# Kernel tuning notes

Hardware: AMD Instinct MI355X
Metric: run time of the kernel (lower is better)

Reference implementation:

```python
import jax, jax.numpy as jnp
import numpy as np

B, S, INPUT_DIM = 8, 2048, 512
D_MODEL, N_LAYERS, OUTPUT_DIM = 1024, 6, 512
LAMBDA_INIT = 0.5


def _sinusoidal_pe(seq_len, d_model):
    # standard sinusoidal positional encoding, added over the sequence dim
    pos = np.arange(seq_len, dtype=np.float32)[:, None]
    div = np.exp(-np.log(10000.0) * np.arange(0, d_model, 2, dtype=np.float32) / d_model)
    pe = np.zeros((seq_len, d_model), dtype=np.float32)
    pe[:, 0::2] = np.sin(pos * div)
    pe[:, 1::2] = np.cos(pos * div)
    return jnp.asarray(pe)


def setup_inputs() -> dict:
    key = jax.random.key(0)
    ks = jax.random.split(key, 10)
    scale = 0.02
    x = jax.random.normal(ks[0], (B, S, INPUT_DIM), dtype=jnp.float32)
    W_in = jax.random.normal(ks[1], (D_MODEL, INPUT_DIM), dtype=jnp.float32) * scale
    b_in = jnp.zeros((D_MODEL,), dtype=jnp.float32)
    W_ctx = jax.random.normal(ks[2], (D_MODEL, D_MODEL), dtype=jnp.float32) * scale
    b_ctx = jnp.zeros((D_MODEL,), dtype=jnp.float32)
    # per-layer in_proj splits: W_q, W_k, W_v each [d_model, d_model]
    Wq = jax.random.normal(ks[3], (N_LAYERS, D_MODEL, D_MODEL), dtype=jnp.float32) * scale
    Wk = jax.random.normal(ks[4], (N_LAYERS, D_MODEL, D_MODEL), dtype=jnp.float32) * scale
    Wv = jax.random.normal(ks[5], (N_LAYERS, D_MODEL, D_MODEL), dtype=jnp.float32) * scale
    W_out = jax.random.normal(ks[6], (OUTPUT_DIM, D_MODEL), dtype=jnp.float32) * scale
    b_out = jnp.zeros((OUTPUT_DIM,), dtype=jnp.float32)
    return {"x": x, "W_in": W_in, "b_in": b_in, "W_ctx": W_ctx, "b_ctx": b_ctx,
            "Wq": Wq, "Wk": Wk, "Wv": Wv, "W_out": W_out, "b_out": b_out}


def _diff_attention(h, W_q, W_k, W_v):
    # h: [B, S, d]; weights used un-transposed, matching X @ W_q in the source
    d = h.shape[-1]
    half = d // 2
    Q = h @ W_q
    K = h @ W_k
    V = h @ W_v
    Q1, Q2 = Q[..., :half], Q[..., half:]
    K1, K2 = K[..., :half], K[..., half:]
    s = 1.0 / jnp.sqrt(jnp.float32(d))
    A1 = jnp.einsum('bqd,bkd->bqk', Q1, K1) * s  # [B, S, S]
    A2 = jnp.einsum('bqd,bkd->bqk', Q2, K2) * s
    scores = jax.nn.softmax(A1, axis=-1) - LAMBDA_INIT * jax.nn.softmax(A2, axis=-1)
    return jnp.einsum('bqk,bkd->bqd', scores, V)


def reference(x, W_in, b_in, W_ctx, b_ctx, Wq, Wk, Wv, W_out, b_out):
    h = x @ W_in.T + b_in            # input_fc
    h = h @ W_ctx.T + b_ctx          # context_embedding
    h = h + _sinusoidal_pe(S, D_MODEL)[None, :, :]
    for i in range(N_LAYERS):
        h = _diff_attention(h, Wq[i], Wk[i], Wv[i])
    return h @ W_out.T + b_out
```

## Files before the change

### kernel.cpp

```cpp
#include <hip/hip_runtime.h>
#include <stdint.h>

typedef unsigned short u16b;
typedef __attribute__((ext_vector_type(8))) __bf16 bf16x8;
typedef __attribute__((ext_vector_type(8))) unsigned short ushort8;
typedef __attribute__((ext_vector_type(4))) float f32x4;

#define B_    8
#define S_    2048
#define DIN_  512
#define DM_   1024
#define NL_   6
#define DOUT_ 512
#define MTOT  (B_ * S_)

__device__ __forceinline__ u16b f2bf(float f) {
  unsigned u = __builtin_bit_cast(unsigned, f);
  u += 0x7fffu + ((u >> 16) & 1u);
  return (u16b)(u >> 16);
}
__device__ __forceinline__ float bf2f(u16b h) {
  return __builtin_bit_cast(float, (unsigned)h << 16);
}

__global__ void pe_kernel(float* __restrict__ pe) {
  int idx = blockIdx.x * 256 + threadIdx.x;
  int s = idx >> 10, d = idx & 1023;
  int j = d >> 1;
  double div = exp(-log(10000.0) * (double)(2 * j) / 1024.0);
  double ang = (double)s * div;
  pe[idx] = (float)((d & 1) ? cos(ang) : sin(ang));
}

__global__ void cvt_bf16(const float* __restrict__ in, u16b* __restrict__ out, long long n) {
  long long i = (long long)blockIdx.x * 256 + threadIdx.x;
  long long st = (long long)gridDim.x * 256;
  for (; i < n; i += st) out[i] = f2bf(in[i]);
}

__global__ __launch_bounds__(256) void tr3v2(const float* __restrict__ q,
                                             const float* __restrict__ k,
                                             const float* __restrict__ v,
                                             u16b* __restrict__ oq, u16b* __restrict__ ok2,
                                             u16b* __restrict__ ov) {
  __shared__ float tile[64 * 65];
  const float* in = blockIdx.z == 0 ? q : (blockIdx.z == 1 ? k : v);
  u16b* out = blockIdx.z == 0 ? oq : (blockIdx.z == 1 ? ok2 : ov);
  int c0 = blockIdx.x * 64, r0 = blockIdx.y * 64;
  int t = threadIdx.x;
#pragma unroll
  for (int i = 0; i < 4; ++i) {
    int id = i * 256 + t;
    int r = id >> 4, cq = (id & 15) * 4;
    float4 val = *(const float4*)&in[(size_t)(r0 + r) * DM_ + c0 + cq];
    tile[r * 65 + cq + 0] = val.x;
    tile[r * 65 + cq + 1] = val.y;
    tile[r * 65 + cq + 2] = val.z;
    tile[r * 65 + cq + 3] = val.w;
  }
  __syncthreads();
#pragma unroll
  for (int i = 0; i < 2; ++i) {
    int id = i * 256 + t;
    int c = id >> 3, rq = (id & 7) * 8;
    ushort8 o;
#pragma unroll
    for (int j = 0; j < 8; ++j) o[j] = f2bf(tile[(rq + j) * 65 + c]);
    *(ushort8*)&out[(size_t)(c0 + c) * DM_ + r0 + rq] = o;
  }
}

__global__ __launch_bounds__(256) void softmax_combine(const float* __restrict__ A1,
                                                       const float* __restrict__ A2,
                                                       u16b* __restrict__ P,
                                                       long long pstride) {
  size_t row = blockIdx.x;
  const float* a1 = A1 + row * 2048;
  const float* a2 = A2 + row * 2048;
  u16b* p = P + row * pstride;
  int t = threadIdx.x, w = t >> 6, lane = t & 63;
  float v1[8], v2[8];
  float m1 = -3.4e38f, m2 = -3.4e38f;
#pragma unroll
  for (int i = 0; i < 8; ++i) {
    v1[i] = a1[i * 256 + t];
    v2[i] = a2[i * 256 + t];
    m1 = fmaxf(m1, v1[i]);
    m2 = fmaxf(m2, v2[i]);
  }
  __shared__ float red1[4], red2[4];
#pragma unroll
  for (int o = 32; o; o >>= 1) {
    m1 = fmaxf(m1, __shfl_xor(m1, o));
    m2 = fmaxf(m2, __shfl_xor(m2, o));
  }
  if (lane == 0) { red1[w] = m1; red2[w] = m2; }
  __syncthreads();
  m1 = fmaxf(fmaxf(red1[0], red1[1]), fmaxf(red1[2], red1[3]));
  m2 = fmaxf(fmaxf(red2[0], red2[1]), fmaxf(red2[2], red2[3]));
  float s1 = 0.f, s2 = 0.f;
#pragma unroll
  for (int i = 0; i < 8; ++i) {
    v1[i] = expf(v1[i] - m1);
    v2[i] = expf(v2[i] - m2);
    s1 += v1[i];
    s2 += v2[i];
  }
#pragma unroll
  for (int o = 32; o; o >>= 1) {
    s1 += __shfl_xor(s1, o);
    s2 += __shfl_xor(s2, o);
  }
  __syncthreads();
  if (lane == 0) { red1[w] = s1; red2[w] = s2; }
  __syncthreads();
  s1 = red1[0] + red1[1] + red1[2] + red1[3];
  s2 = red2[0] + red2[1] + red2[2] + red2[3];
  float i1 = 1.0f / s1, i2 = 0.5f / s2;
#pragma unroll
  for (int i = 0; i < 8; ++i)
    p[i * 256 + t] = f2bf(v1[i] * i1 - v2[i] * i2);
}

__global__ __launch_bounds__(256) void softmax_full(u16b* __restrict__ A1b,
                                                    const u16b* __restrict__ A2b) {
  size_t ro = (size_t)blockIdx.x * S_;
  u16b* a1 = A1b + ro;
  const u16b* a2 = A2b + ro;
  int t = threadIdx.x, w = t >> 6, lane = t & 63;
  ushort8 x1 = *(const ushort8*)&a1[t * 8];
  ushort8 x2 = *(const ushort8*)&a2[t * 8];
  float v1[8], v2[8];
  float m1 = -3.4e38f, m2 = -3.4e38f;
#pragma unroll
  for (int i = 0; i < 8; ++i) {
    v1[i] = bf2f(x1[i]);
    v2[i] = bf2f(x2[i]);
    m1 = fmaxf(m1, v1[i]);
    m2 = fmaxf(m2, v2[i]);
  }
  __shared__ float red1[4], red2[4];
#pragma unroll
  for (int o = 32; o; o >>= 1) {
    m1 = fmaxf(m1, __shfl_xor(m1, o));
    m2 = fmaxf(m2, __shfl_xor(m2, o));
  }
  if (lane == 0) { red1[w] = m1; red2[w] = m2; }
  __syncthreads();
  m1 = fmaxf(fmaxf(red1[0], red1[1]), fmaxf(red1[2], red1[3]));
  m2 = fmaxf(fmaxf(red2[0], red2[1]), fmaxf(red2[2], red2[3]));
  float s1 = 0.f, s2 = 0.f;
#pragma unroll
  for (int i = 0; i < 8; ++i) {
    v1[i] = expf(v1[i] - m1);
    v2[i] = expf(v2[i] - m2);
    s1 += v1[i];
    s2 += v2[i];
  }
#pragma unroll
  for (int o = 32; o; o >>= 1) {
    s1 += __shfl_xor(s1, o);
    s2 += __shfl_xor(s2, o);
  }
  __syncthreads();
  if (lane == 0) { red1[w] = s1; red2[w] = s2; }
  __syncthreads();
  s1 = red1[0] + red1[1] + red1[2] + red1[3];
  s2 = red2[0] + red2[1] + red2[2] + red2[3];
  float i1 = 1.0f / s1, i2 = 0.5f / s2;
  ushort8 outv;
#pragma unroll
  for (int i = 0; i < 8; ++i) outv[i] = f2bf(v1[i] * i1 - v2[i] * i2);
  *(ushort8*)&a1[t * 8] = outv;
}

#define GEPI_BF16      0
#define GEPI_BIAS      1
#define GEPI_BIAS_PE   2
#define GEPI_F32SCALE  3
#define GEPI_F32BIAS   4
#define GEPI_BF16_VT   5
#define GEPI_BF16SCALE 6
#define GEPI_QKV       7

template <int EPI>
__global__ __launch_bounds__(256) void gemm_nt(
    const u16b* __restrict__ A, long long sAr, long long sAb,
    const u16b* __restrict__ Bt, long long sBr, long long sBb,
    void* __restrict__ Cv, long long sCr, long long sCb,
    int K, const float* __restrict__ bias, const float* __restrict__ pe, float alpha) {
  __shared__ __align__(16) u16b smem[16384];
  u16b* As = smem;
  u16b* Bs = smem + 8192;
  const int z = blockIdx.z;
  const u16b* Ab = A + (size_t)z * sAb;
  const u16b* Bb = Bt + (size_t)z * sBb;
  const int m0 = blockIdx.x * 128, n0 = blockIdx.y * 128;
  const int t = threadIdx.x;
  const int w = t >> 6, lane = t & 63;
  const int wr = w >> 1, wc = w & 1;
  const int lr = lane & 15, g0 = lane >> 4;

  f32x4 acc[4][4] = {};

  const int nkt = K >> 6;
  for (int kt = 0; kt < nkt; ++kt) {
#pragma unroll
    for (int i = 0; i < 4; ++i) {
      int c = i * 256 + t;
      int r = c >> 3, cc = c & 7;
      int gc = cc ^ (r & 7);
      const u16b* ga = Ab + (size_t)(m0 + r) * sAr + kt * 64 + gc * 8;
      const u16b* gb = Bb + (size_t)(n0 + r) * sBr + kt * 64 + gc * 8;
      u16b* la = &As[(i * 256 + w * 64) * 8];
      u16b* lb = &Bs[(i * 256 + w * 64) * 8];
      __builtin_amdgcn_global_load_lds((__attribute__((address_space(1))) void*)ga,
                                       (__attribute__((address_space(3))) void*)la, 16, 0, 0);
      __builtin_amdgcn_global_load_lds((__attribute__((address_space(1))) void*)gb,
                                       (__attribute__((address_space(3))) void*)lb, 16, 0, 0);
    }
    __syncthreads();
#pragma unroll
    for (int kk = 0; kk < 2; ++kk) {
      bf16x8 af[4], bfr[4];
#pragma unroll
      for (int m = 0; m < 4; ++m) {
        int r = wr * 64 + m * 16 + lr;
        int sidx = (kk * 4 + g0) ^ (r & 7);
        af[m] = *(const bf16x8*)&As[(r * 8 + sidx) * 8];
      }
#pragma unroll
      for (int n = 0; n < 4; ++n) {
        int r = wc * 64 + n * 16 + lr;
        int sidx = (kk * 4 + g0) ^ (r & 7);
        bfr[n] = *(const bf16x8*)&Bs[(r * 8 + sidx) * 8];
      }
#pragma unroll
      for (int m = 0; m < 4; ++m)
#pragma unroll
        for (int n = 0; n < 4; ++n)
          acc[m][n] = __builtin_amdgcn_mfma_f32_16x16x32_bf16(af[m], bfr[n], acc[m][n], 0, 0, 0);
    }
    __syncthreads();
  }

  u16b* Ch = (u16b*)Cv;
  float* Cf = (float*)Cv;
  const size_t cb = (size_t)z * sCb;
#pragma unroll
  for (int m = 0; m < 4; ++m) {
#pragma unroll
    for (int j = 0; j < 4; ++j) {
      int r = m0 + wr * 64 + m * 16 + g0 * 4 + j;
      size_t ro = cb + (size_t)r * sCr;
#pragma unroll
      for (int n = 0; n < 4; ++n) {
        int c = n0 + wc * 64 + n * 16 + lr;
        float v = acc[m][n][j];
        if constexpr (EPI == GEPI_BF16) Ch[ro + c] = f2bf(v);
        else if constexpr (EPI == GEPI_BIAS) Ch[ro + c] = f2bf(v + bias[c]);
        else if constexpr (EPI == GEPI_BIAS_PE)
          Ch[ro + c] = f2bf(v + bias[c] + pe[(size_t)(r & (S_ - 1)) * DM_ + c]);
        else if constexpr (EPI == GEPI_F32SCALE) Cf[ro + c] = v * alpha;
        else Cf[ro + c] = v + bias[c];
      }
    }
  }
}

template <int EPI>
__global__ __launch_bounds__(512, 1) void gemm8(
    const u16b* __restrict__ A, long long sAr, long long sAb, long long sAb2,
    const u16b* __restrict__ Bt, long long sBr, long long sBb, long long sBb2,
    void* __restrict__ Cv, long long sCr, long long sCb, long long sCb2,
    int K, const float* __restrict__ bias, const float* __restrict__ pe, float alpha) {
  extern __shared__ __align__(16) u16b lds[];
  const int z = blockIdx.z;
  const u16b* Ab = A + (size_t)(z >> 1) * sAb2 + (size_t)(z & 1) * sAb;
  const u16b* Bb = Bt + (size_t)(z >> 1) * sBb2 + (size_t)(z & 1) * sBb;
  const int m0 = blockIdx.x * 256, n0 = blockIdx.y * 256;
  const int t = threadIdx.x;
  const int wid = t >> 6, lane = t & 63;
  const int wr = wid >> 2, wc = wid & 3;
  const int lr = lane & 15, g0 = lane >> 4;

  f32x4 acc[8][4] = {};
  const int nkt = K >> 6;

  auto stage = [&](int kt, int buf) {
    u16b* bufA = lds + buf * 32768;
    u16b* bufB = bufA + 16384;
#pragma unroll
    for (int i = 0; i < 4; ++i) {
      int id = i * 512 + t;
      int r = id >> 3, cc = id & 7;
      int gc = cc ^ (r & 7);
      const u16b* ga = Ab + (size_t)(m0 + r) * sAr + kt * 64 + gc * 8;
      const u16b* gb = Bb + (size_t)(n0 + r) * sBr + kt * 64 + gc * 8;
      u16b* la = bufA + (i * 512 + wid * 64) * 8;
      u16b* lb = bufB + (i * 512 + wid * 64) * 8;
      __builtin_amdgcn_global_load_lds((__attribute__((address_space(1))) void*)ga,
                                       (__attribute__((address_space(3))) void*)la, 16, 0, 0);
      __builtin_amdgcn_global_load_lds((__attribute__((address_space(1))) void*)gb,
                                       (__attribute__((address_space(3))) void*)lb, 16, 0, 0);
    }
  };

  stage(0, 0);
  __builtin_amdgcn_sched_barrier(0);
  asm volatile("s_waitcnt vmcnt(0)" ::: "memory");
  __builtin_amdgcn_sched_barrier(0);
  __builtin_amdgcn_s_barrier();
  __builtin_amdgcn_sched_barrier(0);

  for (int kt = 0; kt < nkt; ++kt) {
    const int cur = kt & 1;
    if (kt + 1 < nkt) stage(kt + 1, cur ^ 1);
    __builtin_amdgcn_sched_barrier(0);
    const u16b* bufA = lds + cur * 32768;
    const u16b* bufB = bufA + 16384;
#pragma unroll
    for (int kk = 0; kk < 2; ++kk) {
      bf16x8 af[8], bfr[4];
#pragma unroll
      for (int m = 0; m < 8; ++m) {
        int r = wr * 128 + m * 16 + lr;
        int sidx = (kk * 4 + g0) ^ (r & 7);
        af[m] = *(const bf16x8*)&bufA[(r * 8 + sidx) * 8];
      }
#pragma unroll
      for (int n = 0; n < 4; ++n) {
        int r = wc * 64 + n * 16 + lr;
        int sidx = (kk * 4 + g0) ^ (r & 7);
        bfr[n] = *(const bf16x8*)&bufB[(r * 8 + sidx) * 8];
      }
      __builtin_amdgcn_s_setprio(1);
#pragma unroll
      for (int m = 0; m < 8; ++m)
#pragma unroll
        for (int n = 0; n < 4; ++n)
          acc[m][n] = __builtin_amdgcn_mfma_f32_16x16x32_bf16(af[m], bfr[n], acc[m][n], 0, 0, 0);
      __builtin_amdgcn_s_setprio(0);
    }
    __builtin_amdgcn_sched_barrier(0);
    asm volatile("s_waitcnt vmcnt(0)" ::: "memory");
    __builtin_amdgcn_sched_barrier(0);
    __builtin_amdgcn_s_barrier();
    __builtin_amdgcn_sched_barrier(0);
  }

  const bool doVT = (EPI == GEPI_BF16_VT) || (EPI == GEPI_QKV && z == 2);
  if (doVT) {
    u16b* tile = lds;
    u16b* vtb = (EPI == GEPI_QKV) ? (u16b*)(void*)pe : (u16b*)Cv;
#pragma unroll
    for (int m = 0; m < 8; ++m)
#pragma unroll
      for (int j = 0; j < 4; ++j) {
        int rl = wr * 128 + m * 16 + g0 * 4 + j;
#pragma unroll
        for (int n = 0; n < 4; ++n) {
          int cl = wc * 64 + n * 16 + lr;
          tile[cl * 256 + (rl ^ ((cl & 7) << 3))] = f2bf(acc[m][n][j]);
        }
      }
    __syncthreads();
    const int batch = m0 >> 11;
    const int r0b = m0 & (S_ - 1);
    u16b* obase = vtb + (size_t)batch * DM_ * S_ + r0b;
#pragma unroll
    for (int it = 0; it < 16; ++it) {
      int id = it * 512 + t;
      int c = id >> 5, rc = id & 31;
      *(bf16x8*)&obase[(size_t)(n0 + c) * S_ + rc * 8] =
          *(const bf16x8*)&tile[c * 256 + ((rc * 8) ^ ((c & 7) << 3))];
    }
    return;
  }

  u16b* Ch = (u16b*)Cv;
  float* Cf = (float*)Cv;
  const size_t cb = (size_t)(z >> 1) * sCb2 + (size_t)(z & 1) * sCb;
#pragma unroll
  for (int m = 0; m < 8; ++m) {
#pragma unroll
    for (int j = 0; j < 4; ++j) {
      int r = m0 + wr * 128 + m * 16 + g0 * 4 + j;
      size_t ro = cb + (size_t)r * sCr;
#pragma unroll
      for (int n = 0; n < 4; ++n) {
        int c = n0 + wc * 64 + n * 16 + lr;
        float v = acc[m][n][j];
        if constexpr (EPI == GEPI_BF16 || EPI == GEPI_QKV) Ch[ro + c] = f2bf(v);
        else if constexpr (EPI == GEPI_BIAS) Ch[ro + c] = f2bf(v + bias[c]);
        else if constexpr (EPI == GEPI_BIAS_PE)
          Ch[ro + c] = f2bf(v + bias[c] + pe[(size_t)(r & (S_ - 1)) * DM_ + c]);
        else if constexpr (EPI == GEPI_F32SCALE) Cf[ro + c] = v * alpha;
        else if constexpr (EPI == GEPI_BF16SCALE) Ch[ro + c] = f2bf(v * alpha);
        else Cf[ro + c] = v + bias[c];
      }
    }
  }
}

extern "C" void kernel_launch(void* const* d_in, const int* in_sizes, int n_in,
                              void* d_out, int out_size, void* d_ws, size_t ws_size,
                              hipStream_t stream) {
  const float* x     = (const float*)d_in[0];
  const float* W_in  = (const float*)d_in[1];
  const float* b_in  = (const float*)d_in[2];
  const float* W_ctx = (const float*)d_in[3];
  const float* b_ctx = (const float*)d_in[4];
  const float* Wq    = (const float*)d_in[5];
  const float* Wk    = (const float*)d_in[6];
  const float* Wv    = (const float*)d_in[7];
  const float* W_out = (const float*)d_in[8];
  const float* b_out = (const float*)d_in[9];
  float* out = (float*)d_out;

  const int LDS8 = 131072;
  hipFuncSetAttribute((const void*)gemm8<GEPI_BF16>,
                      hipFuncAttributeMaxDynamicSharedMemorySize, LDS8);
  hipFuncSetAttribute((const void*)gemm8<GEPI_BIAS>,
                      hipFuncAttributeMaxDynamicSharedMemorySize, LDS8);
  hipFuncSetAttribute((const void*)gemm8<GEPI_BIAS_PE>,
                      hipFuncAttributeMaxDynamicSharedMemorySize, LDS8);
  hipFuncSetAttribute((const void*)gemm8<GEPI_QKV>,
                      hipFuncAttributeMaxDynamicSharedMemorySize, LDS8);
  hipFuncSetAttribute((const void*)gemm8<GEPI_BF16SCALE>,
                      hipFuncAttributeMaxDynamicSharedMemorySize, LDS8);

  const size_t SZ_A12 = (size_t)2 * S_ * S_ * 4;
  const size_t SZ_PF  = (size_t)B_ * S_ * S_ * 2;
  const size_t SZ_H   = (size_t)MTOT * DM_ * 2;
  const size_t SZ_WIN = (size_t)DM_ * DIN_ * 2;
  const size_t SZ_WX  = (size_t)DM_ * DM_ * 2;
  const size_t SZ_WO  = (size_t)DOUT_ * DM_ * 2;
  const size_t SZ_WL  = (size_t)3 * DM_ * DM_ * 2;
  const size_t SLACK  = 65536;
  const size_t needB = SZ_A12 + SZ_PF + 4 * SZ_H + SZ_WO + SZ_WL + SLACK;
  const size_t needC = SZ_A12 + 4 * SZ_H + SZ_WIN + SZ_WX + SZ_WO + SZ_WL + SLACK;
  bool fullP = ws_size >= needB;
  if (ws_size < needC) return;

  char* wsp = (char*)d_ws;
  size_t off = 0;
  auto alloc = [&](size_t bytes) -> void* {
    void* p = wsp + off;
    off += (bytes + 255) & ~(size_t)255;
    return p;
  };
  u16b* Pfull = fullP ? (u16b*)alloc(SZ_PF) : nullptr;
  float* A12  = (float*)alloc(SZ_A12);
  u16b* hbuf  = (u16b*)alloc(SZ_H);
  u16b* qbuf  = (u16b*)alloc(SZ_H);
  u16b* kbuf  = (u16b*)alloc(SZ_H);
  u16b* vtb   = (u16b*)alloc(SZ_H);
  u16b *winb, *wctxb;
  if (fullP) {
    winb  = (u16b*)Pfull;
    wctxb = (u16b*)((char*)Pfull + SZ_WIN);
  } else {
    winb  = (u16b*)alloc(SZ_WIN);
    wctxb = (u16b*)alloc(SZ_WX);
  }
  u16b* woutb = (u16b*)alloc(SZ_WO);
  u16b* wTl   = (u16b*)alloc(SZ_WL);

  u16b* xbf = (u16b*)A12;
  float* pe = (float*)((char*)A12 + (size_t)MTOT * DIN_ * 2);
  float* A1f = A12;
  float* A2f = A12 + (size_t)S_ * S_;
  u16b* A2u  = (u16b*)A12;

  const size_t WSTEP = (size_t)DM_ * DM_;
  u16b* wqTl = wTl;
  u16b* wkTl = wTl + WSTEP;
  u16b* wvTl = wTl + 2 * WSTEP;

  dim3 blk(256);

  pe_kernel<<<dim3((S_ * DM_) / 256), blk, 0, stream>>>(pe);
  cvt_bf16<<<dim3(2048), blk, 0, stream>>>(x, xbf, (long long)MTOT * DIN_);
  cvt_bf16<<<dim3(512), blk, 0, stream>>>(W_in, winb, (long long)DM_ * DIN_);
  cvt_bf16<<<dim3(1024), blk, 0, stream>>>(W_ctx, wctxb, (long long)DM_ * DM_);
  cvt_bf16<<<dim3(512), blk, 0, stream>>>(W_out, woutb, (long long)DOUT_ * DM_);

  gemm8<GEPI_BIAS><<<dim3(MTOT / 256, DM_ / 256, 1), dim3(512), LDS8, stream>>>(
      xbf, DIN_, 0, 0, winb, DIN_, 0, 0, qbuf, DM_, 0, 0, DIN_, b_in, nullptr, 1.0f);
  gemm8<GEPI_BIAS_PE><<<dim3(MTOT / 256, DM_ / 256, 1), dim3(512), LDS8, stream>>>(
      qbuf, DM_, 0, 0, wctxb, DM_, 0, 0, hbuf, DM_, 0, 0, DM_, b_ctx, pe, 1.0f);

  for (int l = 0; l < NL_; ++l) {
    tr3v2<<<dim3(DM_ / 64, DM_ / 64, 3), blk, 0, stream>>>(
        Wq + (size_t)l * WSTEP, Wk + (size_t)l * WSTEP, Wv + (size_t)l * WSTEP,
        wqTl, wkTl, wvTl);
    gemm8<GEPI_QKV><<<dim3(MTOT / 256, DM_ / 256, 3), dim3(512), LDS8, stream>>>(
        hbuf, DM_, 0, 0, wqTl, DM_, (long long)WSTEP, 2 * (long long)WSTEP,
        qbuf, DM_, (long long)(kbuf - qbuf), 0, DM_, nullptr, (const float*)vtb, 1.0f);

    if (fullP) {
      gemm8<GEPI_BF16SCALE><<<dim3(S_ / 256, S_ / 256, 16), dim3(512), LDS8, stream>>>(
          qbuf, DM_, DM_ / 2, (long long)S_ * DM_,
          kbuf, DM_, DM_ / 2, (long long)S_ * DM_,
          Pfull, S_, (long long)(A2u - Pfull), (long long)S_ * S_,
          DM_ / 2, nullptr, nullptr, 0.03125f);
      softmax_full<<<dim3(MTOT), blk, 0, stream>>>(Pfull, A2u);
      gemm8<GEPI_BF16><<<dim3(S_ / 256, DM_ / 256, B_), dim3(512), LDS8, stream>>>(
          Pfull, S_, (long long)S_ * S_, 2 * (long long)S_ * S_,
          vtb, S_, (long long)DM_ * S_, 2 * (long long)DM_ * S_,
          hbuf, DM_, (long long)S_ * DM_, 2 * (long long)S_ * DM_,
          S_, nullptr, nullptr, 1.0f);
    } else {
      for (int b = 0; b < B_; ++b) {
        const u16b* qb = qbuf + (size_t)b * S_ * DM_;
        const u16b* kb = kbuf + (size_t)b * S_ * DM_;
        gemm_nt<GEPI_F32SCALE><<<dim3(S_ / 128, S_ / 128, 2), blk, 0, stream>>>(
            qb, DM_, DM_ / 2, kb, DM_, DM_ / 2,
            A1f, S_, (long long)S_ * S_, DM_ / 2, nullptr, nullptr, 0.03125f);
        softmax_combine<<<dim3(S_), blk, 0, stream>>>(A1f, A2f, (u16b*)A1f, 2 * S_);
        gemm_nt<GEPI_BF16><<<dim3(S_ / 128, DM_ / 128, 1), blk, 0, stream>>>(
            (u16b*)A1f, 2 * S_, 0, vtb + (size_t)b * DM_ * S_, S_, 0,
            hbuf + (size_t)b * S_ * DM_, DM_, 0, S_, nullptr, nullptr, 1.0f);
      }
    }
  }

  gemm_nt<GEPI_F32BIAS><<<dim3(MTOT / 128, DOUT_ / 128, 1), blk, 0, stream>>>(
      hbuf, DM_, 0, woutb, DM_, 0, out, DOUT_, 0, DM_, b_out, nullptr, 1.0f);
}
```

Measured before the change: 1.767 ms.

## Fold input and context projections into a single precomputed weight and bias

The two back-to-back linear layers (input_fc then context_embedding) are merged algebraically. A small GEMM first computes W_eff = W_ctx·W_in and a fused bias b = W_ctx·b_in + b_ctx, then a single large GEMM with K=512 replaces the two large GEMMs (K=512 and K=1024). This removes roughly two thirds of the embedding-stage FLOPs and one full activation write and read. The folded weight is rounded to bf16, which changes rounding slightly. The PE kernel also switches from double to float math, which is cheaper but slightly less precise.

Result: no change. 1.780 ms (+0.7%).

```diff
diff --git a/kernel.cpp b/kernel.cpp
--- a/kernel.cpp
+++ b/kernel.cpp
@@ -27,15 +27,42 @@
   int idx = blockIdx.x * 256 + threadIdx.x;
   int s = idx >> 10, d = idx & 1023;
   int j = d >> 1;
-  double div = exp(-log(10000.0) * (double)(2 * j) / 1024.0);
-  double ang = (double)s * div;
-  pe[idx] = (float)((d & 1) ? cos(ang) : sin(ang));
+  float div = expf(-9.2103404f * (float)(2 * j) * (1.0f / 1024.0f));
+  float ang = (float)s * div;
+  pe[idx] = (d & 1) ? cosf(ang) : sinf(ang);
 }
 
 __global__ void cvt_bf16(const float* __restrict__ in, u16b* __restrict__ out, long long n) {
   long long i = (long long)blockIdx.x * 256 + threadIdx.x;
   long long st = (long long)gridDim.x * 256;
   for (; i < n; i += st) out[i] = f2bf(in[i]);
+}
+
+__global__ __launch_bounds__(256) void trg_f32_bf16(const float* __restrict__ in,
+                                                    u16b* __restrict__ out, int R, int C) {
+  __shared__ float tile[64 * 65];
+  int c0 = blockIdx.x * 64, r0 = blockIdx.y * 64;
+  int t = threadIdx.x;
+#pragma unroll
+  for (int i = 0; i < 4; ++i) {
+    int id = i * 256 + t;
+    int r = id >> 4, cq = (id & 15) * 4;
+    float4 val = *(const float4*)&in[(size_t)(r0 + r) * C + c0 + cq];
+    tile[r * 65 + cq + 0] = val.x;
+    tile[r * 65 + cq + 1] = val.y;
+    tile[r * 65 + cq + 2] = val.z;
+    tile[r * 65 + cq + 3] = val.w;
+  }
+  __syncthreads();
+#pragma unroll
+  for (int i = 0; i < 2; ++i) {
+    int id = i * 256 + t;
+    int c = id >> 3, rq = (id & 7) * 8;
+    ushort8 o;
+#pragma unroll
+    for (int j = 0; j < 8; ++j) o[j] = f2bf(tile[(rq + j) * 65 + c]);
+    *(ushort8*)&out[(size_t)(c0 + c) * R + r0 + rq] = o;
+  }
 }
 
 __global__ __launch_bounds__(256) void tr3v2(const float* __restrict__ q,
@@ -68,6 +95,17 @@
     for (int j = 0; j < 8; ++j) o[j] = f2bf(tile[(rq + j) * 65 + c]);
     *(ushort8*)&out[(size_t)(c0 + c) * DM_ + r0 + rq] = o;
   }
+}
+
+__global__ __launch_bounds__(256) void bias_fold(const float* __restrict__ b_in,
+                                                 const float* __restrict__ W_ctx,
+                                                 const float* __restrict__ b_ctx,
+                                                 float* __restrict__ bc2) {
+  int n = blockIdx.x * 256 + threadIdx.x;
+  float s = b_ctx[n];
+  const float* row = W_ctx + (size_t)n * DM_;
+  for (int k = 0; k < DM_; ++k) s += b_in[k] * row[k];
+  bc2[n] = s;
 }
 
 __global__ __launch_bounds__(256) void softmax_combine(const float* __restrict__ A1,
@@ -421,8 +459,6 @@
   const int LDS8 = 131072;
   hipFuncSetAttribute((const void*)gemm8<GEPI_BF16>,
                       hipFuncAttributeMaxDynamicSharedMemorySize, LDS8);
-  hipFuncSetAttribute((const void*)gemm8<GEPI_BIAS>,
-                      hipFuncAttributeMaxDynamicSharedMemorySize, LDS8);
   hipFuncSetAttribute((const void*)gemm8<GEPI_BIAS_PE>,
                       hipFuncAttributeMaxDynamicSharedMemorySize, LDS8);
   hipFuncSetAttribute((const void*)gemm8<GEPI_QKV>,
@@ -433,13 +469,14 @@
   const size_t SZ_A12 = (size_t)2 * S_ * S_ * 4;
   const size_t SZ_PF  = (size_t)B_ * S_ * S_ * 2;
   const size_t SZ_H   = (size_t)MTOT * DM_ * 2;
-  const size_t SZ_WIN = (size_t)DM_ * DIN_ * 2;
-  const size_t SZ_WX  = (size_t)DM_ * DM_ * 2;
+  const size_t SZ_WX  = (size_t)DM_ * DM_ * 4 / 2;
+  const size_t SZ_WT  = (size_t)DIN_ * DM_ * 2;
+  const size_t SZ_WE  = (size_t)DM_ * DIN_ * 2;
   const size_t SZ_WO  = (size_t)DOUT_ * DM_ * 2;
   const size_t SZ_WL  = (size_t)3 * DM_ * DM_ * 2;
   const size_t SLACK  = 65536;
   const size_t needB = SZ_A12 + SZ_PF + 4 * SZ_H + SZ_WO + SZ_WL + SLACK;
-  const size_t needC = SZ_A12 + 4 * SZ_H + SZ_WIN + SZ_WX + SZ_WO + SZ_WL + SLACK;
+  const size_t needC = SZ_A12 + 4 * SZ_H + SZ_WX + SZ_WT + SZ_WE + SZ_WO + SZ_WL + SLACK;
   bool fullP = ws_size >= needB;
   if (ws_size < needC) return;
 
@@ -456,16 +493,19 @@
   u16b* qbuf  = (u16b*)alloc(SZ_H);
   u16b* kbuf  = (u16b*)alloc(SZ_H);
   u16b* vtb   = (u16b*)alloc(SZ_H);
-  u16b *winb, *wctxb;
+  u16b *wctxb, *winT, *weff;
   if (fullP) {
-    winb  = (u16b*)Pfull;
-    wctxb = (u16b*)((char*)Pfull + SZ_WIN);
+    wctxb = (u16b*)Pfull;
+    winT  = (u16b*)((char*)Pfull + SZ_WX);
+    weff  = (u16b*)((char*)Pfull + SZ_WX + SZ_WT);
   } else {
-    winb  = (u16b*)alloc(SZ_WIN);
     wctxb = (u16b*)alloc(SZ_WX);
+    winT  = (u16b*)alloc(SZ_WT);
+    weff  = (u16b*)alloc(SZ_WE);
   }
   u16b* woutb = (u16b*)alloc(SZ_WO);
   u16b* wTl   = (u16b*)alloc(SZ_WL);
+  float* bc2  = (float*)alloc(DM_ * 4);
 
   u16b* xbf = (u16b*)A12;
   float* pe = (float*)((char*)A12 + (size_t)MTOT * DIN_ * 2);
@@ -482,14 +522,16 @@
 
   pe_kernel<<<dim3((S_ * DM_) / 256), blk, 0, stream>>>(pe);
   cvt_bf16<<<dim3(2048), blk, 0, stream>>>(x, xbf, (long long)MTOT * DIN_);
-  cvt_bf16<<<dim3(512), blk, 0, stream>>>(W_in, winb, (long long)DM_ * DIN_);
   cvt_bf16<<<dim3(1024), blk, 0, stream>>>(W_ctx, wctxb, (long long)DM_ * DM_);
+  trg_f32_bf16<<<dim3(DIN_ / 64, DM_ / 64), blk, 0, stream>>>(W_in, winT, DM_, DIN_);
   cvt_bf16<<<dim3(512), blk, 0, stream>>>(W_out, woutb, (long long)DOUT_ * DM_);
 
-  gemm8<GEPI_BIAS><<<dim3(MTOT / 256, DM_ / 256, 1), dim3(512), LDS8, stream>>>(
-      xbf, DIN_, 0, 0, winb, DIN_, 0, 0, qbuf, DM_, 0, 0, DIN_, b_in, nullptr, 1.0f);
+  gemm_nt<GEPI_BF16><<<dim3(DM_ / 128, DIN_ / 128, 1), blk, 0, stream>>>(
+      wctxb, DM_, 0, winT, DM_, 0, weff, DIN_, 0, DM_, nullptr, nullptr, 1.0f);
+  bias_fold<<<dim3(DM_ / 256), blk, 0, stream>>>(b_in, W_ctx, b_ctx, bc2);
+
   gemm8<GEPI_BIAS_PE><<<dim3(MTOT / 256, DM_ / 256, 1), dim3(512), LDS8, stream>>>(
-      qbuf, DM_, 0, 0, wctxb, DM_, 0, 0, hbuf, DM_, 0, 0, DM_, b_ctx, pe, 1.0f);
+      xbf, DIN_, 0, 0, weff, DIN_, 0, 0, hbuf, DM_, 0, 0, DIN_, bc2, pe, 1.0f);
 
   for (int l = 0; l < NL_; ++l) {
     tr3v2<<<dim3(DM_ / 64, DM_ / 64, 3), blk, 0, stream>>>(
```
